# Kernel tuning notes

Measured on AMD Instinct MI355X. Metric: run time of the kernel, lower is better.

Reference implementation:

```python
import jax, jax.numpy as jnp
import numpy as np

D_MODEL = 1024
N_HEADS = 16
D_HEAD = D_MODEL // N_HEADS  # 64
M = int(round(D_HEAD * np.log(D_HEAD)))  # 266 random features, per source
KERNEL_EPS = 1e-4


def setup_inputs() -> dict:
    key = jax.random.key(0)
    ks = jax.random.split(key, 12)
    B, L = 2, 2048
    sc = 1.0 / np.sqrt(D_MODEL)
    return {
        "query": jax.random.normal(ks[0], (B, L, D_MODEL), jnp.float32),
        "key_": jax.random.normal(ks[1], (B, L, D_MODEL), jnp.float32),
        "value": jax.random.normal(ks[2], (B, L, D_MODEL), jnp.float32),
        "Wq": jax.random.normal(ks[3], (D_MODEL, D_MODEL), jnp.float32) * sc,
        "bq": jnp.zeros((D_MODEL,), jnp.float32),
        "Wk": jax.random.normal(ks[4], (D_MODEL, D_MODEL), jnp.float32) * sc,
        "bk": jnp.zeros((D_MODEL,), jnp.float32),
        "Wv": jax.random.normal(ks[5], (D_MODEL, D_MODEL), jnp.float32) * sc,
        "bv": jnp.zeros((D_MODEL,), jnp.float32),
        "Wo": jax.random.normal(ks[6], (D_MODEL, D_MODEL), jnp.float32) * sc,
        "bo": jnp.zeros((D_MODEL,), jnp.float32),
        "random_features": jax.random.normal(ks[7], (M, D_HEAD), jnp.float32),
    }


def _split_heads(x):
    # [B,L,d_model] -> [B,H,L,D]
    B, L, _ = x.shape
    return x.reshape(B, L, N_HEADS, D_HEAD).transpose(0, 2, 1, 3)


def _favor_projected(q, k, rf):
    # q,k: [B,H,L,D]; rf: [M,D]. Faithful to get_projected_queries_and_keys (kernel_type='exp').
    q = q / (D_MODEL ** 0.25)
    k = k / (D_MODEL ** 0.25)
    pq = jnp.einsum('bhld,md->bhlm', q, rf)
    pk = jnp.einsum('bhld,md->bhlm', k, rf)
    h_q = -0.5 * jnp.sum(q * q, axis=-1, keepdims=True)  # [B,H,L,1]
    h_k = -0.5 * jnp.sum(k * k, axis=-1, keepdims=True)
    q_stab = jnp.max(h_q, axis=-1, keepdims=True)  # == h_q (last dim is 1), as in source
    k_stab = jnp.max(h_k)  # global scalar, as in source
    q_ker = jnp.exp(h_q + (pq - q_stab))
    k_ker = jnp.exp(h_k + (pk - k_stab))
    c = M ** (-0.5)
    return c * (q_ker + KERNEL_EPS), c * (k_ker + KERNEL_EPS)


def _causal_favor(qp, kp, v):
    # qp,kp: [L,B,H,M]; v: [L,B,H,D]. Prefix-sum linear attention.
    # Denominator: q_prime[i] . cumsum(k_prime)[i]
    denom = jnp.einsum('lbhm,lbhm->lbh', qp, jnp.cumsum(kp, axis=0))

    # Numerator: recurrent scan carrying S = sum_j k'_j v_j^T  ([B,H,M,D])
    def step(S, inp):
        q_t, k_t, v_t = inp
        S = S + k_t[..., :, None] * v_t[..., None, :]
        out_t = jnp.einsum('bhmd,bhm->bhd', S, q_t)
        return S, out_t

    S0 = jnp.zeros(kp.shape[1:] + (v.shape[-1],), kp.dtype)
    _, num = jax.lax.scan(step, S0, (qp, kp, v))  # num: [L,B,H,D]
    return num / denom[..., None]


def reference(query, key_, value, Wq, bq, Wk, bk, Wv, bv, Wo, bo, random_features):
    B, L, _ = query.shape
    q = _split_heads(query @ Wq + bq)   # [B,H,L,D]
    k = _split_heads(key_ @ Wk + bk)
    v = _split_heads(value @ Wv + bv)
    q_prime, k_prime = _favor_projected(q, k, random_features)  # [B,H,L,M]
    # Causal path operates sequence-first: [L,B,H,*]
    qp = q_prime.transpose(2, 0, 1, 3)
    kp = k_prime.transpose(2, 0, 1, 3)
    vt = v.transpose(2, 0, 1, 3)
    out = _causal_favor(qp, kp, vt)               # [L,B,H,D]
    ctx = out.transpose(1, 0, 2, 3).reshape(B, L, D_MODEL)
    return ctx @ Wo + bo
```

## Files before the change

kernel.cpp:

```cpp
#include <hip/hip_runtime.h>
#include <hip/hip_bf16.h>

#define BATCH 2
#define SEQ 2048
#define DMODEL 1024
#define NH 16
#define HD 64
#define NRF 266
#define NRFP 288
#define CHK 128
#define NCH 16
#define NBH 32
#define NROWS 4096

constexpr float SCAL = 0.17677669529663687f;
constexpr float SCAL2 = 0.03125f;
constexpr float LN_CNORM = -2.7917480361965505f;
constexpr float CKEPS = 6.131393094576169e-6f;

typedef short bf16x8 __attribute__((ext_vector_type(8)));
typedef float f32x4 __attribute__((ext_vector_type(4)));

__device__ __forceinline__ short f2bs(float v) {
  __hip_bfloat16 h = __float2bfloat16(v);
  return *reinterpret_cast<short*>(&h);
}
__device__ __forceinline__ float bs2f(short s) {
  __hip_bfloat16 h;
  *reinterpret_cast<short*>(&h) = s;
  return __bfloat162float(h);
}
__device__ __forceinline__ void gload_lds16(const void* g, void* l) {
  __builtin_amdgcn_global_load_lds(
      (const __attribute__((address_space(1))) void*)g,
      (__attribute__((address_space(3))) void*)l, 16, 0, 0);
}
__device__ __forceinline__ unsigned f2ord(float f) {
  unsigned u = __float_as_uint(f);
  return (u & 0x80000000u) ? ~u : (u | 0x80000000u);
}
__device__ __forceinline__ float ord2f(unsigned e) {
  return (e & 0x80000000u) ? __uint_as_float(e & 0x7fffffffu)
                           : __uint_as_float(~e);
}

__global__ __launch_bounds__(256) void cvt3_kernel(const float* __restrict__ q,
                                                   const float* __restrict__ k,
                                                   const float* __restrict__ v,
                                                   short* __restrict__ out) {
  int z = blockIdx.y;
  const float* x = (z == 0) ? q : (z == 1) ? k : v;
  short* y = out + (size_t)z * NROWS * DMODEL;
  int i = (blockIdx.x * 256 + threadIdx.x) * 8;
  float4 a = *(const float4*)&x[i];
  float4 b = *(const float4*)&x[i + 4];
  bf16x8 o;
  o[0] = f2bs(a.x); o[1] = f2bs(a.y); o[2] = f2bs(a.z); o[3] = f2bs(a.w);
  o[4] = f2bs(b.x); o[5] = f2bs(b.y); o[6] = f2bs(b.z); o[7] = f2bs(b.w);
  *(bf16x8*)&y[i] = o;
}

__global__ __launch_bounds__(256) void rf_pad_bf16(const float* __restrict__ rf,
                                                   short* __restrict__ rfb,
                                                   unsigned* __restrict__ kord) {
  int idx = blockIdx.x * 256 + threadIdx.x;
  rfb[idx] = (idx < NRF * HD) ? f2bs(rf[idx] * SCAL) : (short)0;
  if (idx == 0) *kord = 0u;
}

__global__ __launch_bounds__(256) void transpose4_bf16(
    const float* __restrict__ Wq, const float* __restrict__ Wk,
    const float* __restrict__ Wv, const float* __restrict__ Wo,
    short* __restrict__ WtBase) {
  __shared__ float t[32][33];
  int z = blockIdx.z;
  const float* W = (z == 0) ? Wq : (z == 1) ? Wk : (z == 2) ? Wv : Wo;
  short* Wt = WtBase + (size_t)z * DMODEL * DMODEL;
  int k0 = blockIdx.y << 5, n0 = blockIdx.x << 5;
  int tx = threadIdx.x & 31, ty = threadIdx.x >> 5;
#pragma unroll
  for (int rr = 0; rr < 4; ++rr) {
    int r = ty + (rr << 3);
    t[r][tx] = W[(size_t)(k0 + r) * DMODEL + n0 + tx];
  }
  __syncthreads();
#pragma unroll
  for (int rr = 0; rr < 4; ++rr) {
    int r = ty + (rr << 3);
    Wt[(size_t)(n0 + r) * DMODEL + k0 + tx] = f2bs(t[tx][r]);
  }
}

template <bool OUTBF>
__device__ __forceinline__ void gemm_core128(const short* __restrict__ A,
                                             const short* __restrict__ Bt,
                                             const float* __restrict__ bias,
                                             void* __restrict__ C, int bm, int bn) {
  __shared__ short As[2][128 * 64];
  __shared__ short Bs[2][128 * 64];
  int tid = threadIdx.x;
  int lane = tid & 63, wid = tid >> 6;
  int wr = wid >> 1, wc = wid & 1;
  int cl = lane & 15, rq = lane >> 4;
  f32x4 acc[4][4];
#pragma unroll
  for (int m = 0; m < 4; ++m)
#pragma unroll
    for (int n = 0; n < 4; ++n) acc[m][n] = f32x4{0.f, 0.f, 0.f, 0.f};

  auto stage = [&](int buf, int k0) {
#pragma unroll
    for (int i = 0; i < 4; ++i) {
      int e = tid * 8 + i * 2048;
      int row = e >> 6;
      int k = (e & 63) ^ ((row & 7) << 3);
      gload_lds16(A + (size_t)(bm + row) * DMODEL + k0 + k,
                  &As[buf][wid * 512 + i * 2048]);
    }
#pragma unroll
    for (int i = 0; i < 4; ++i) {
      int e = tid * 8 + i * 2048;
      int row = e >> 6;
      int k = (e & 63) ^ ((row & 7) << 3);
      gload_lds16(Bt + (size_t)(bn + row) * DMODEL + k0 + k,
                  &Bs[buf][wid * 512 + i * 2048]);
    }
  };

  stage(0, 0);
#pragma unroll 2
  for (int t = 0; t < 16; ++t) {
    int cur = t & 1;
    if (t < 15) {
      stage(cur ^ 1, (t + 1) * 64);
      asm volatile("s_waitcnt vmcnt(8)" ::: "memory");
    } else {
      asm volatile("s_waitcnt vmcnt(0)" ::: "memory");
    }
    __builtin_amdgcn_s_barrier();
    asm volatile("" ::: "memory");
    const short* curA = &As[cur][0];
    const short* curB = &Bs[cur][0];
#pragma unroll
    for (int ks = 0; ks < 2; ++ks) {
      int kb = ks * 32 + (rq << 3);
      bf16x8 af[4], bfv[4];
#pragma unroll
      for (int mf = 0; mf < 4; ++mf) {
        int row = wr * 64 + mf * 16 + cl;
        af[mf] = *(const bf16x8*)&curA[row * 64 + (kb ^ ((row & 7) << 3))];
      }
#pragma unroll
      for (int nf = 0; nf < 4; ++nf) {
        int row = wc * 64 + nf * 16 + cl;
        bfv[nf] = *(const bf16x8*)&curB[row * 64 + (kb ^ ((row & 7) << 3))];
      }
#pragma unroll
      for (int mf = 0; mf < 4; ++mf)
#pragma unroll
        for (int nf = 0; nf < 4; ++nf)
          acc[mf][nf] = __builtin_amdgcn_mfma_f32_16x16x32_bf16(af[mf], bfv[nf],
                                                                acc[mf][nf], 0, 0, 0);
    }
    __builtin_amdgcn_s_barrier();
    asm volatile("" ::: "memory");
  }
  int rbase = bm + wr * 64 + (rq << 2);
  int cbase = bn + wc * 64 + cl;
#pragma unroll
  for (int nf = 0; nf < 4; ++nf) {
    int col = cbase + nf * 16;
    float bv = bias[col];
#pragma unroll
    for (int mf = 0; mf < 4; ++mf)
#pragma unroll
      for (int r = 0; r < 4; ++r) {
        int row = rbase + mf * 16 + r;
        float v = acc[mf][nf][r] + bv;
        if (OUTBF)
          ((short*)C)[(size_t)row * DMODEL + col] = f2bs(v);
        else
          ((float*)C)[(size_t)row * DMODEL + col] = v;
      }
  }
}

template <bool OUTBF>
__device__ __forceinline__ void gemm_core64(const short* __restrict__ A,
                                            const short* __restrict__ Bt,
                                            const float* __restrict__ bias,
                                            void* __restrict__ C, int bm, int bn) {
  __shared__ short As[2][128 * 64];
  __shared__ short Bs[2][64 * 64];
  int tid = threadIdx.x;
  int lane = tid & 63, wid = tid >> 6;
  int wr = wid >> 1, wc = wid & 1;
  f32x4 acc[4][2];
#pragma unroll
  for (int m = 0; m < 4; ++m)
#pragma unroll
    for (int n = 0; n < 2; ++n) acc[m][n] = f32x4{0.f, 0.f, 0.f, 0.f};

  auto stage = [&](int buf, int k0) {
#pragma unroll
    for (int i = 0; i < 4; ++i) {
      int e = tid * 8 + i * 2048;
      int row = e >> 6;
      int k = (e & 63) ^ ((row & 7) << 3);
      gload_lds16(A + (size_t)(bm + row) * DMODEL + k0 + k,
                  &As[buf][wid * 512 + i * 2048]);
    }
#pragma unroll
    for (int i = 0; i < 2; ++i) {
      int e = tid * 8 + i * 2048;
      int row = e >> 6;
      int k = (e & 63) ^ ((row & 7) << 3);
      gload_lds16(Bt + (size_t)(bn + row) * DMODEL + k0 + k,
                  &Bs[buf][wid * 512 + i * 2048]);
    }
  };

  stage(0, 0);
#pragma unroll 2
  for (int t = 0; t < 16; ++t) {
    int cur = t & 1;
    if (t < 15) {
      stage(cur ^ 1, (t + 1) * 64);
      asm volatile("s_waitcnt vmcnt(6)" ::: "memory");
    } else {
      asm volatile("s_waitcnt vmcnt(0)" ::: "memory");
    }
    __builtin_amdgcn_s_barrier();
    asm volatile("" ::: "memory");
    const short* curA = &As[cur][0];
    const short* curB = &Bs[cur][0];
#pragma unroll
    for (int ks = 0; ks < 2; ++ks) {
      int kb = ks * 32 + ((lane >> 4) << 3);
      bf16x8 af[4], bfv[2];
#pragma unroll
      for (int mf = 0; mf < 4; ++mf) {
        int row = wr * 64 + mf * 16 + (lane & 15);
        af[mf] = *(const bf16x8*)&curA[row * 64 + (kb ^ ((row & 7) << 3))];
      }
#pragma unroll
      for (int nf = 0; nf < 2; ++nf) {
        int row = wc * 32 + nf * 16 + (lane & 15);
        bfv[nf] = *(const bf16x8*)&curB[row * 64 + (kb ^ ((row & 7) << 3))];
      }
#pragma unroll
      for (int mf = 0; mf < 4; ++mf)
#pragma unroll
        for (int nf = 0; nf < 2; ++nf)
          acc[mf][nf] = __builtin_amdgcn_mfma_f32_16x16x32_bf16(af[mf], bfv[nf],
                                                                acc[mf][nf], 0, 0, 0);
    }
    __builtin_amdgcn_s_barrier();
    asm volatile("" ::: "memory");
  }
  int rbase = bm + wr * 64 + ((lane >> 4) << 2);
  int cbase = bn + wc * 32 + (lane & 15);
#pragma unroll
  for (int nf = 0; nf < 2; ++nf) {
    int col = cbase + nf * 16;
    float bv = bias[col];
#pragma unroll
    for (int mf = 0; mf < 4; ++mf)
#pragma unroll
      for (int r = 0; r < 4; ++r) {
        int row = rbase + mf * 16 + r;
        float v = acc[mf][nf][r] + bv;
        if (OUTBF)
          ((short*)C)[(size_t)row * DMODEL + col] = f2bs(v);
        else
          ((float*)C)[(size_t)row * DMODEL + col] = v;
      }
  }
}

__global__ __launch_bounds__(256) void gemm_qkv3(
    const short* __restrict__ Abase, const short* __restrict__ WtBase,
    const float* __restrict__ bq, const float* __restrict__ bk,
    const float* __restrict__ bv, short* __restrict__ OutBase) {
  int z = blockIdx.z;
  const short* A = Abase + (size_t)z * NROWS * DMODEL;
  const short* Bt = WtBase + (size_t)z * DMODEL * DMODEL;
  const float* bias = (z == 0) ? bq : (z == 1) ? bk : bv;
  short* C = OutBase + (size_t)z * NROWS * DMODEL;
  int bid = blockIdx.x + (blockIdx.y << 3);
  int swz = ((bid & 7) << 5) + (bid >> 3);
  int bn = (swz & 7) << 7;
  int bm = (swz >> 3) << 7;
  gemm_core128<true>(A, Bt, bias, C, bm, bn);
}

__global__ __launch_bounds__(256) void gemm_out(const short* __restrict__ A,
                                                const short* __restrict__ Bt,
                                                const float* __restrict__ bias,
                                                float* __restrict__ C) {
  int bid = blockIdx.x + (blockIdx.y << 4);
  int swz = ((bid & 7) << 6) + (bid >> 3);
  int bn = (swz & 15) << 6;
  int bm = (swz >> 4) << 7;
  gemm_core64<false>(A, Bt, bias, C, bm, bn);
}

__global__ __launch_bounds__(256) void hk_kernel(const short* __restrict__ Kb,
                                                 float* __restrict__ hkbuf,
                                                 unsigned* __restrict__ kord) {
  int tid = threadIdx.x;
  int rloc = tid >> 4, h = tid & 15;
  int n = blockIdx.x * 16 + rloc;
  const short* p = Kb + (size_t)n * DMODEL + h * HD;
  float ss = 0.f;
#pragma unroll
  for (int g = 0; g < 8; ++g) {
    bf16x8 v = *(const bf16x8*)(p + g * 8);
#pragma unroll
    for (int e = 0; e < 8; ++e) {
      float x = bs2f(v[e]);
      ss += x * x;
    }
  }
  float hkv = -0.5f * SCAL2 * ss;
  int b = n >> 11, l = n & (SEQ - 1);
  hkbuf[((size_t)(b * NH + h)) * SEQ + l] = hkv;
  __shared__ float red[256];
  red[tid] = hkv;
  __syncthreads();
  for (int s = 128; s > 0; s >>= 1) {
    if (tid < s) red[tid] = fmaxf(red[tid], red[tid + s]);
    __syncthreads();
  }
  if (tid == 0) atomicMax(kord, f2ord(red[0]));
}

__global__ __launch_bounds__(256, 1) void featmap_mfma(
    const short* __restrict__ Qproj, const short* __restrict__ Kproj,
    const short* __restrict__ rfb, const float* __restrict__ hkbuf,
    const unsigned* __restrict__ kord, short* __restrict__ Qp,
    short* __restrict__ Kp) {
  __shared__ short smem[26624];
  __shared__ float hks[128];
  short* As = smem;
  short* Bs = smem + 8192;
  int isK = blockIdx.z;
  const short* X = isK ? Kproj : Qproj;
  short* O = isK ? Kp : Qp;
  int bh = blockIdx.y, b = bh >> 4, h = bh & 15;
  int l0 = blockIdx.x << 7;
  int tid = threadIdx.x, lane = tid & 63, wid = tid >> 6;
  int cl = lane & 15, rq = lane >> 4;

#pragma unroll
  for (int i = 0; i < 4; ++i) {
    int e = tid * 8 + i * 2048;
    int row = e >> 6;
    int k = (e & 63) ^ ((row & 7) << 3);
    gload_lds16(X + ((size_t)b * SEQ + l0 + row) * DMODEL + h * HD + k,
                &As[wid * 512 + i * 2048]);
  }
#pragma unroll
  for (int i = 0; i < 9; ++i) {
    int e = tid * 8 + i * 2048;
    int row = e >> 6;
    int k = (e & 63) ^ ((row & 7) << 3);
    gload_lds16(rfb + row * HD + k, &Bs[wid * 512 + i * 2048]);
  }
  if (isK) {
    float ksv = ord2f(*kord);
    if (tid < 128)
      hks[tid] = hkbuf[(size_t)bh * SEQ + l0 + tid] - ksv + LN_CNORM;
  }
  __syncthreads();

  int i0 = wid * 32;
  f32x4 acc[2][18];
#pragma unroll
  for (int m = 0; m < 2; ++m)
#pragma unroll
    for (int n = 0; n < 18; ++n) acc[m][n] = f32x4{0.f, 0.f, 0.f, 0.f};
#pragma unroll
  for (int ks = 0; ks < 2; ++ks) {
    int kb = ks * 32 + (rq << 3);
    int swz = (cl & 7) << 3;
    bf16x8 af[2];
#pragma unroll
    for (int mf = 0; mf < 2; ++mf) {
      int row = i0 + mf * 16 + cl;
      af[mf] = *(const bf16x8*)&As[row * 64 + (kb ^ swz)];
    }
#pragma unroll
    for (int nf = 0; nf < 18; ++nf) {
      int brow = nf * 16 + cl;
      bf16x8 bv = *(const bf16x8*)&Bs[brow * 64 + (kb ^ swz)];
#pragma unroll
      for (int mf = 0; mf < 2; ++mf)
        acc[mf][nf] = __builtin_amdgcn_mfma_f32_16x16x32_bf16(af[mf], bv,
                                                              acc[mf][nf], 0, 0, 0);
    }
  }

  short* Ps = smem;
#pragma unroll
  for (int hf = 0; hf < 2; ++hf) {
    __syncthreads();
#pragma unroll
    for (int mf = 0; mf < 2; ++mf)
#pragma unroll
      for (int r = 0; r < 4; ++r) {
        int rl = i0 + mf * 16 + (rq << 2) + r;
        float addk = isK ? hks[rl] : LN_CNORM;
#pragma unroll
        for (int nf2 = 0; nf2 < 9; ++nf2) {
          int m = hf * 144 + nf2 * 16 + cl;
          float v = acc[mf][hf * 9 + nf2][r] + addk;
          float o = (m < NRF) ? (__expf(v) + CKEPS) : 0.f;
          Ps[rl * 152 + nf2 * 16 + cl] = f2bs(o);
        }
      }
    __syncthreads();
#pragma unroll
    for (int it = 0; it < 9; ++it) {
      int idx = tid + it * 256;
      int row = idx / 18, ch = idx - row * 18;
      bf16x8 val = *(const bf16x8*)&Ps[row * 152 + ch * 8];
      *(bf16x8*)&O[((size_t)bh * SEQ + l0 + row) * NRFP + hf * 144 + ch * 8] = val;
    }
  }
}

__global__ __launch_bounds__(256) void chunksum_mfma(
    const short* __restrict__ Kp, const short* __restrict__ Vb,
    short* __restrict__ Schunk, float* __restrict__ ksum) {
  constexpr int ST = 70;
  __shared__ short KT[NRFP * ST];
  __shared__ short VT[HD * ST];
  int c = blockIdx.x, bh = blockIdx.y;
  int b = bh >> 4, h = bh & 15;
  int tid = threadIdx.x, lane = tid & 63, wv = tid >> 6;
  int cl = lane & 15, rq = lane >> 4;
  int irow = tid >> 2;
  int mq = tid & 3;
  size_t rowb = (size_t)bh * SEQ + (size_t)c * CHK;

  f32x4 acc[18];
#pragma unroll
  for (int m = 0; m < 18; ++m) acc[m] = f32x4{0.f, 0.f, 0.f, 0.f};
  float k1 = 0.f, k2 = 0.f;

  for (int hf = 0; hf < 2; ++hf) {
    __syncthreads();
    const short* Krow = Kp + (rowb + hf * 64 + irow) * NRFP;
#pragma unroll
    for (int cg = 0; cg < 9; ++cg) {
      int m0 = cg * 32 + mq * 8;
      bf16x8 v = *(const bf16x8*)(Krow + m0);
#pragma unroll
      for (int e = 0; e < 8; ++e) KT[(m0 + e) * ST + irow] = v[e];
    }
    const short* Vrow =
        Vb + ((size_t)b * SEQ + (size_t)c * CHK + hf * 64 + irow) * DMODEL + h * HD;
    {
      int d0 = mq * 16;
      bf16x8 v0 = *(const bf16x8*)(Vrow + d0);
      bf16x8 v1 = *(const bf16x8*)(Vrow + d0 + 8);
#pragma unroll
      for (int e = 0; e < 8; ++e) VT[(d0 + e) * ST + irow] = v0[e];
#pragma unroll
      for (int e = 0; e < 8; ++e) VT[(d0 + 8 + e) * ST + irow] = v1[e];
    }
    __syncthreads();
#pragma unroll
    for (int ks = 0; ks < 2; ++ks) {
      int kb = ks * 32 + rq * 8;
      bf16x8 bv = *(const bf16x8*)&VT[(wv * 16 + cl) * ST + kb];
#pragma unroll
      for (int mf = 0; mf < 18; ++mf) {
        bf16x8 av = *(const bf16x8*)&KT[(mf * 16 + cl) * ST + kb];
        acc[mf] = __builtin_amdgcn_mfma_f32_16x16x32_bf16(av, bv, acc[mf], 0, 0, 0);
      }
    }
    {
      const short* r1 = &KT[tid * ST];
#pragma unroll
      for (int g = 0; g < 8; ++g) {
        bf16x8 v = *(const bf16x8*)(r1 + g * 8);
#pragma unroll
        for (int e = 0; e < 8; ++e) k1 += bs2f(v[e]);
      }
      if (tid < 10) {
        const short* r2 = &KT[(256 + tid) * ST];
#pragma unroll
        for (int g = 0; g < 8; ++g) {
          bf16x8 v = *(const bf16x8*)(r2 + g * 8);
#pragma unroll
          for (int e = 0; e < 8; ++e) k2 += bs2f(v[e]);
        }
      }
    }
  }
  size_t sbase = ((size_t)bh * NCH + c) * (size_t)(NRFP * HD);
  size_t kbase = ((size_t)bh * NCH + c) * (size_t)NRF;
#pragma unroll
  for (int mf = 0; mf < 18; ++mf)
#pragma unroll
    for (int r = 0; r < 4; ++r) {
      int m = mf * 16 + rq * 4 + r;
      Schunk[sbase + (size_t)m * HD + wv * 16 + cl] = f2bs(acc[mf][r]);
    }
  if (tid < NRF) ksum[kbase + tid] = k1;
  if (tid < 10) ksum[kbase + 256 + tid] = k2;
}

__global__ __launch_bounds__(256) void prefix_all(const short* __restrict__ Sc,
                                                  short* __restrict__ Sp,
                                                  float* __restrict__ ksum) {
  int bh = blockIdx.y;
  if (blockIdx.x == 72) {
    for (int m = threadIdx.x; m < NRF; m += 256) {
      size_t base = (size_t)bh * NCH * NRF + m;
      float a = 0.f;
#pragma unroll
      for (int c = 0; c < NCH; ++c) {
        size_t idx = base + (size_t)c * NRF;
        float v = ksum[idx];
        ksum[idx] = a;
        a += v;
      }
    }
    return;
  }
  int e = blockIdx.x * 256 + threadIdx.x;
  size_t base = (size_t)bh * NCH * (NRFP * HD) + e;
  float a = 0.f;
#pragma unroll
  for (int c = 0; c < NCH; ++c) {
    size_t idx = base + (size_t)c * (NRFP * HD);
    float v = bs2f(Sc[idx]);
    Sp[idx] = f2bs(a);
    a += v;
  }
}

__global__ __launch_bounds__(256) void attn_mfma(
    const short* __restrict__ Qp, const short* __restrict__ Kp,
    const short* __restrict__ Vb, const short* __restrict__ Sp,
    const float* __restrict__ ksum, short* __restrict__ ctxb) {
  constexpr int PST = 136;
  constexpr int BST = 290;
  __shared__ short Vt[64 * PST];
  __shared__ short BsPl[64 * BST];
  __shared__ float ks[272];
  __shared__ float den[128];
  int c = blockIdx.x, bh = blockIdx.y;
  int b = bh >> 4, h = bh & 15;
  int tid = threadIdx.x, lane = tid & 63, wid = tid >> 6;
  int cl = lane & 15, rq = lane >> 4;
  size_t rowb = (size_t)bh * SEQ + (size_t)c * CHK;

  {
    int jj = tid >> 3, d0 = (tid & 7) << 3;
#pragma unroll
    for (int jt = 0; jt < 4; ++jt) {
      int j = jj + jt * 32;
      bf16x8 v = *(const bf16x8*)(Vb + ((size_t)b * SEQ + (size_t)c * CHK + j) * DMODEL +
                                  h * HD + d0);
#pragma unroll
      for (int e = 0; e < 8; ++e) Vt[(d0 + e) * PST + j] = v[e];
    }
  }
  const short* Spb = Sp + ((size_t)bh * NCH + c) * (size_t)(NRFP * HD);
  for (int idx = tid; idx < NRFP * HD; idx += 256) {
    int m = idx >> 6, d = idx & 63;
    BsPl[d * BST + m] = Spb[idx];
  }
  const float* ksb = ksum + ((size_t)bh * NCH + c) * (size_t)NRF;
  for (int idx = tid; idx < NRF; idx += 256) ks[idx] = ksb[idx];
  __syncthreads();

  int i0 = wid * 32;
  const short* Arow = Qp + (rowb + i0) * NRFP;
  const short* Krow = Kp + rowb * NRFP;
  f32x4 accI[2][4];
  f32x4 accP[2][8];
#pragma unroll
  for (int m = 0; m < 2; ++m) {
#pragma unroll
    for (int n = 0; n < 4; ++n) accI[m][n] = f32x4{0.f, 0.f, 0.f, 0.f};
#pragma unroll
    for (int n = 0; n < 8; ++n) accP[m][n] = f32x4{0.f, 0.f, 0.f, 0.f};
  }
#pragma unroll
  for (int k9 = 0; k9 < 9; ++k9) {
    int kb = k9 * 32 + (rq << 3);
    bf16x8 af[2];
#pragma unroll
    for (int mf = 0; mf < 2; ++mf)
      af[mf] = *(const bf16x8*)(Arow + (size_t)(mf * 16 + cl) * NRFP + kb);
#pragma unroll
    for (int nf = 0; nf < 4; ++nf) {
      bf16x8 bv = *(const bf16x8*)&BsPl[(nf * 16 + cl) * BST + kb];
#pragma unroll
      for (int mf = 0; mf < 2; ++mf)
        accI[mf][nf] = __builtin_amdgcn_mfma_f32_16x16x32_bf16(af[mf], bv,
                                                               accI[mf][nf], 0, 0, 0);
    }
#pragma unroll
    for (int nf = 0; nf < 8; ++nf) {
      bf16x8 bv = *(const bf16x8*)(Krow + (size_t)(nf * 16 + cl) * NRFP + kb);
#pragma unroll
      for (int mf = 0; mf < 2; ++mf)
        accP[mf][nf] = __builtin_amdgcn_mfma_f32_16x16x32_bf16(af[mf], bv,
                                                               accP[mf][nf], 0, 0, 0);
    }
  }
  {
    int r = tid >> 1, half = tid & 1;
    const short* qr = Qp + (rowb + r) * NRFP;
    float s = 0.f;
    int m0 = half * 133;
    for (int m = m0; m < m0 + 133; ++m) s += bs2f(qr[m]) * ks[m];
    s += __shfl_xor(s, 1);
    if (!half) den[r] = s;
  }
  __syncthreads();

#pragma unroll
  for (int mf = 0; mf < 2; ++mf)
#pragma unroll
    for (int r = 0; r < 4; ++r) {
      int rl = mf * 16 + (rq << 2) + r;
      int row = i0 + rl;
      float dsum = 0.f;
#pragma unroll
      for (int nf = 0; nf < 8; ++nf) {
        int col = nf * 16 + cl;
        float v = (col > row) ? 0.f : accP[mf][nf][r];
        dsum += v;
        BsPl[wid * 32 * PST + rl * PST + col] = f2bs(v);
      }
      dsum += __shfl_xor(dsum, 1);
      dsum += __shfl_xor(dsum, 2);
      dsum += __shfl_xor(dsum, 4);
      dsum += __shfl_xor(dsum, 8);
      if (cl == 0) den[row] += dsum;
    }
  __syncthreads();

  f32x4 pacc[2][4];
#pragma unroll
  for (int m = 0; m < 2; ++m)
#pragma unroll
    for (int n = 0; n < 4; ++n) pacc[m][n] = f32x4{0.f, 0.f, 0.f, 0.f};
#pragma unroll
  for (int kk = 0; kk < 4; ++kk) {
    int kb = kk * 32 + (rq << 3);
    bf16x8 paf[2];
#pragma unroll
    for (int mf = 0; mf < 2; ++mf)
      paf[mf] = *(const bf16x8*)&BsPl[wid * 32 * PST + (mf * 16 + cl) * PST + kb];
#pragma unroll
    for (int nf = 0; nf < 4; ++nf) {
      bf16x8 bv = *(const bf16x8*)&Vt[(nf * 16 + cl) * PST + kb];
#pragma unroll
      for (int mf = 0; mf < 2; ++mf)
        pacc[mf][nf] = __builtin_amdgcn_mfma_f32_16x16x32_bf16(paf[mf], bv,
                                                               pacc[mf][nf], 0, 0, 0);
    }
  }
#pragma unroll
  for (int mf = 0; mf < 2; ++mf)
#pragma unroll
    for (int r = 0; r < 4; ++r) {
      int row = i0 + mf * 16 + (rq << 2) + r;
      float inv = 1.0f / den[row];
      size_t ob = ((size_t)b * SEQ + (size_t)c * CHK + row) * DMODEL + h * HD;
#pragma unroll
      for (int nf = 0; nf < 4; ++nf) {
        int d = nf * 16 + cl;
        float v = (accI[mf][nf][r] + pacc[mf][nf][r]) * inv;
        ctxb[ob + d] = f2bs(v);
      }
    }
}

extern "C" void kernel_launch(void* const* d_in, const int* in_sizes, int n_in,
                              void* d_out, int out_size, void* d_ws, size_t ws_size,
                              hipStream_t stream) {
  (void)in_sizes; (void)n_in; (void)out_size;
  const float* query = (const float*)d_in[0];
  const float* key_  = (const float*)d_in[1];
  const float* value = (const float*)d_in[2];
  const float* Wq = (const float*)d_in[3];
  const float* bq = (const float*)d_in[4];
  const float* Wk = (const float*)d_in[5];
  const float* bk = (const float*)d_in[6];
  const float* Wv = (const float*)d_in[7];
  const float* bv = (const float*)d_in[8];
  const float* Wo = (const float*)d_in[9];
  const float* bo = (const float*)d_in[10];
  const float* rf = (const float*)d_in[11];

  constexpr size_t SZ_INBF = (size_t)NROWS * DMODEL * 2;
  constexpr size_t SZ_QP   = (size_t)NBH * SEQ * NRFP * 2;
  constexpr size_t SZ_WT   = (size_t)DMODEL * DMODEL * 2;
  constexpr size_t SZ_SCH  = (size_t)NBH * NCH * NRFP * HD * 2;
  constexpr size_t SZ_KS   = (size_t)NBH * NCH * NRF * 4;
  constexpr size_t SZ_HK   = (size_t)NBH * SEQ * 4;
  constexpr size_t SZ_RFB  = (size_t)NRFP * HD * 2;

  constexpr size_t O_QP   = 0;
  constexpr size_t O_KP   = O_QP + SZ_QP;
  constexpr size_t O_WT   = O_KP + SZ_QP;
  constexpr size_t O_QPR  = O_WT + 4 * SZ_WT;
  constexpr size_t O_SCH  = O_QPR + 3 * SZ_INBF;
  constexpr size_t O_SPR  = O_SCH + SZ_SCH;
  constexpr size_t O_KSUM = O_SPR + SZ_SCH;
  constexpr size_t O_HK   = O_KSUM + SZ_KS;
  constexpr size_t O_KST  = O_HK + SZ_HK;
  constexpr size_t O_CTXB = O_KST + 256;
  constexpr size_t O_RFB  = O_CTXB + SZ_INBF;
  constexpr size_t O_END  = O_RFB + SZ_RFB;
  if (ws_size < O_END) return;

  char* w = (char*)d_ws;
  short* Qbf  = (short*)(w + O_QP);
  short* Qp   = (short*)(w + O_QP);
  short* Kp   = (short*)(w + O_KP);
  short* WtB  = (short*)(w + O_WT);
  short* QprB = (short*)(w + O_QPR);
  short* Kpr  = (short*)(w + O_QPR + SZ_INBF);
  short* Vpr  = (short*)(w + O_QPR + 2 * SZ_INBF);
  short* Sch  = (short*)(w + O_SCH);
  short* Spr  = (short*)(w + O_SPR);
  float* ksum = (float*)(w + O_KSUM);
  float* hkbuf = (float*)(w + O_HK);
  unsigned* kord = (unsigned*)(w + O_KST);
  short* ctxb = (short*)(w + O_CTXB);
  short* rfb  = (short*)(w + O_RFB);

  constexpr int NEL = NROWS * DMODEL;
  cvt3_kernel<<<dim3(NEL / 2048, 3), 256, 0, stream>>>(query, key_, value, Qbf);
  transpose4_bf16<<<dim3(32, 32, 4), 256, 0, stream>>>(Wq, Wk, Wv, Wo, WtB);
  rf_pad_bf16<<<(NRFP * HD) / 256, 256, 0, stream>>>(rf, rfb, kord);
  gemm_qkv3<<<dim3(8, 32, 3), 256, 0, stream>>>(Qbf, WtB, bq, bk, bv, QprB);
  hk_kernel<<<256, 256, 0, stream>>>(Kpr, hkbuf, kord);
  featmap_mfma<<<dim3(SEQ / 128, NBH, 2), 256, 0, stream>>>(QprB, Kpr, rfb, hkbuf,
                                                            kord, Qp, Kp);
  chunksum_mfma<<<dim3(NCH, NBH), 256, 0, stream>>>(Kp, Vpr, Sch, ksum);
  prefix_all<<<dim3(73, NBH), 256, 0, stream>>>(Sch, Spr, ksum);
  attn_mfma<<<dim3(NCH, NBH), 256, 0, stream>>>(Qp, Kp, Vpr, Spr, ksum, ctxb);
  gemm_out<<<dim3(16, 32), 256, 0, stream>>>(ctxb, WtB + 3 * (size_t)DMODEL * DMODEL,
                                             bo, (float*)d_out);
}
```

Baseline: 184.7 us.

## Store chunk states transposed, async-load to swizzled LDS, compute denominator via MFMA

Result: no change. 184.1 us, median of 2 (-0.3%).

```diff
diff --git a/kernel.cpp b/kernel.cpp
--- a/kernel.cpp
+++ b/kernel.cpp
@@ -8,6 +8,7 @@
 #define HD 64
 #define NRF 266
 #define NRFP 288
+#define SROW 320
 #define CHK 128
 #define NCH 16
 #define NBH 32
@@ -432,7 +433,7 @@
 
 __global__ __launch_bounds__(256) void chunksum_mfma(
     const short* __restrict__ Kp, const short* __restrict__ Vb,
-    short* __restrict__ Schunk, float* __restrict__ ksum) {
+    short* __restrict__ Sct, float* __restrict__ ksum) {
   constexpr int ST = 70;
   __shared__ short KT[NRFP * ST];
   __shared__ short VT[HD * ST];
@@ -500,65 +501,81 @@
       }
     }
   }
-  size_t sbase = ((size_t)bh * NCH + c) * (size_t)(NRFP * HD);
+  size_t sbase = ((size_t)bh * NCH + c) * (size_t)(HD * SROW);
+  int d = wv * 16 + cl;
+#pragma unroll
+  for (int mf = 0; mf < 18; ++mf) {
+    short4 o4 = make_short4(f2bs(acc[mf][0]), f2bs(acc[mf][1]),
+                            f2bs(acc[mf][2]), f2bs(acc[mf][3]));
+    *(short4*)&Sct[sbase + (size_t)d * SROW + mf * 16 + rq * 4] = o4;
+  }
+  {
+    int dz = tid >> 2, off = NRFP + ((tid & 3) << 3);
+    bf16x8 z = {0, 0, 0, 0, 0, 0, 0, 0};
+    *(bf16x8*)&Sct[sbase + (size_t)dz * SROW + off] = z;
+  }
   size_t kbase = ((size_t)bh * NCH + c) * (size_t)NRF;
-#pragma unroll
-  for (int mf = 0; mf < 18; ++mf)
-#pragma unroll
-    for (int r = 0; r < 4; ++r) {
-      int m = mf * 16 + rq * 4 + r;
-      Schunk[sbase + (size_t)m * HD + wv * 16 + cl] = f2bs(acc[mf][r]);
-    }
   if (tid < NRF) ksum[kbase + tid] = k1;
   if (tid < 10) ksum[kbase + 256 + tid] = k2;
 }
 
-__global__ __launch_bounds__(256) void prefix_all(const short* __restrict__ Sc,
-                                                  short* __restrict__ Sp,
-                                                  float* __restrict__ ksum) {
+__global__ __launch_bounds__(256) void prefix_all(const short* __restrict__ Sct,
+                                                  short* __restrict__ Spt,
+                                                  const float* __restrict__ ksum,
+                                                  short* __restrict__ ksb) {
   int bh = blockIdx.y;
-  if (blockIdx.x == 72) {
-    for (int m = threadIdx.x; m < NRF; m += 256) {
-      size_t base = (size_t)bh * NCH * NRF + m;
-      float a = 0.f;
-#pragma unroll
-      for (int c = 0; c < NCH; ++c) {
-        size_t idx = base + (size_t)c * NRF;
-        float v = ksum[idx];
-        ksum[idx] = a;
-        a += v;
+  if (blockIdx.x == 80) {
+    for (int m = threadIdx.x; m < NRFP; m += 256) {
+      if (m < NRF) {
+        size_t base = (size_t)bh * NCH * NRF + m;
+        float a = 0.f;
+#pragma unroll
+        for (int c = 0; c < NCH; ++c) {
+          float v = ksum[base + (size_t)c * NRF];
+          ksb[((size_t)bh * NCH + c) * NRFP + m] = f2bs(a);
+          a += v;
+        }
+      } else {
+#pragma unroll
+        for (int c = 0; c < NCH; ++c)
+          ksb[((size_t)bh * NCH + c) * NRFP + m] = 0;
       }
     }
     return;
   }
   int e = blockIdx.x * 256 + threadIdx.x;
-  size_t base = (size_t)bh * NCH * (NRFP * HD) + e;
   float a = 0.f;
 #pragma unroll
   for (int c = 0; c < NCH; ++c) {
-    size_t idx = base + (size_t)c * (NRFP * HD);
-    float v = bs2f(Sc[idx]);
-    Sp[idx] = f2bs(a);
+    size_t idx = ((size_t)bh * NCH + c) * (size_t)(HD * SROW) + e;
+    float v = bs2f(Sct[idx]);
+    Spt[idx] = f2bs(a);
     a += v;
   }
 }
 
 __global__ __launch_bounds__(256) void attn_mfma(
     const short* __restrict__ Qp, const short* __restrict__ Kp,
-    const short* __restrict__ Vb, const short* __restrict__ Sp,
-    const float* __restrict__ ksum, short* __restrict__ ctxb) {
+    const short* __restrict__ Vb, const short* __restrict__ Spt,
+    const short* __restrict__ ksb, short* __restrict__ ctxb) {
   constexpr int PST = 136;
-  constexpr int BST = 290;
   __shared__ short Vt[64 * PST];
-  __shared__ short BsPl[64 * BST];
-  __shared__ float ks[272];
-  __shared__ float den[128];
+  __shared__ short SP[64 * SROW];
   int c = blockIdx.x, bh = blockIdx.y;
   int b = bh >> 4, h = bh & 15;
   int tid = threadIdx.x, lane = tid & 63, wid = tid >> 6;
   int cl = lane & 15, rq = lane >> 4;
   size_t rowb = (size_t)bh * SEQ + (size_t)c * CHK;
 
+  const short* sg = Spt + ((size_t)bh * NCH + c) * (size_t)(HD * SROW);
+#pragma unroll
+  for (int i = 0; i < 10; ++i) {
+    int o = tid * 8 + i * 2048;
+    int d = o / SROW;
+    int m = o - d * SROW;
+    int ms = m ^ ((d & 7) << 3);
+    gload_lds16(sg + (size_t)d * SROW + ms, &SP[wid * 512 + i * 2048]);
+  }
   {
     int jj = tid >> 3, d0 = (tid & 7) << 3;
 #pragma unroll
@@ -570,24 +587,20 @@
       for (int e = 0; e < 8; ++e) Vt[(d0 + e) * PST + j] = v[e];
     }
   }
-  const short* Spb = Sp + ((size_t)bh * NCH + c) * (size_t)(NRFP * HD);
-  for (int idx = tid; idx < NRFP * HD; idx += 256) {
-    int m = idx >> 6, d = idx & 63;
-    BsPl[d * BST + m] = Spb[idx];
-  }
-  const float* ksb = ksum + ((size_t)bh * NCH + c) * (size_t)NRF;
-  for (int idx = tid; idx < NRF; idx += 256) ks[idx] = ksb[idx];
   __syncthreads();
 
   int i0 = wid * 32;
   const short* Arow = Qp + (rowb + i0) * NRFP;
   const short* Krow = Kp + rowb * NRFP;
+  const short* krow = ksb + ((size_t)bh * NCH + c) * NRFP;
   f32x4 accI[2][4];
+  f32x4 accD[2];
   f32x4 accP[2][8];
 #pragma unroll
   for (int m = 0; m < 2; ++m) {
 #pragma unroll
     for (int n = 0; n < 4; ++n) accI[m][n] = f32x4{0.f, 0.f, 0.f, 0.f};
+    accD[m] = f32x4{0.f, 0.f, 0.f, 0.f};
 #pragma unroll
     for (int n = 0; n < 8; ++n) accP[m][n] = f32x4{0.f, 0.f, 0.f, 0.f};
   }
@@ -598,9 +611,15 @@
 #pragma unroll
     for (int mf = 0; mf < 2; ++mf)
       af[mf] = *(const bf16x8*)(Arow + (size_t)(mf * 16 + cl) * NRFP + kb);
+    bf16x8 bvD = {0, 0, 0, 0, 0, 0, 0, 0};
+    if (cl == 0) bvD = *(const bf16x8*)(krow + kb);
+#pragma unroll
+    for (int mf = 0; mf < 2; ++mf)
+      accD[mf] = __builtin_amdgcn_mfma_f32_16x16x32_bf16(af[mf], bvD, accD[mf], 0, 0, 0);
 #pragma unroll
     for (int nf = 0; nf < 4; ++nf) {
-      bf16x8 bv = *(const bf16x8*)&BsPl[(nf * 16 + cl) * BST + kb];
+      int row = nf * 16 + cl;
+      bf16x8 bv = *(const bf16x8*)&SP[row * SROW + (kb ^ ((cl & 7) << 3))];
 #pragma unroll
       for (int mf = 0; mf < 2; ++mf)
         accI[mf][nf] = __builtin_amdgcn_mfma_f32_16x16x32_bf16(af[mf], bv,
@@ -615,17 +634,9 @@
                                                                accP[mf][nf], 0, 0, 0);
     }
   }
-  {
-    int r = tid >> 1, half = tid & 1;
-    const short* qr = Qp + (rowb + r) * NRFP;
-    float s = 0.f;
-    int m0 = half * 133;
-    for (int m = m0; m < m0 + 133; ++m) s += bs2f(qr[m]) * ks[m];
-    s += __shfl_xor(s, 1);
-    if (!half) den[r] = s;
-  }
   __syncthreads();
 
+  float dtot[2][4];
 #pragma unroll
   for (int mf = 0; mf < 2; ++mf)
 #pragma unroll
@@ -638,13 +649,14 @@
         int col = nf * 16 + cl;
         float v = (col > row) ? 0.f : accP[mf][nf][r];
         dsum += v;
-        BsPl[wid * 32 * PST + rl * PST + col] = f2bs(v);
+        SP[wid * 32 * PST + rl * PST + col] = f2bs(v);
       }
       dsum += __shfl_xor(dsum, 1);
       dsum += __shfl_xor(dsum, 2);
       dsum += __shfl_xor(dsum, 4);
       dsum += __shfl_xor(dsum, 8);
-      if (cl == 0) den[row] += dsum;
+      float dden = __shfl(accD[mf][r], lane & 48);
+      dtot[mf][r] = dden + dsum;
     }
   __syncthreads();
 
@@ -659,7 +671,7 @@
     bf16x8 paf[2];
 #pragma unroll
     for (int mf = 0; mf < 2; ++mf)
-      paf[mf] = *(const bf16x8*)&BsPl[wid * 32 * PST + (mf * 16 + cl) * PST + kb];
+      paf[mf] = *(const bf16x8*)&SP[wid * 32 * PST + (mf * 16 + cl) * PST + kb];
 #pragma unroll
     for (int nf = 0; nf < 4; ++nf) {
       bf16x8 bv = *(const bf16x8*)&Vt[(nf * 16 + cl) * PST + kb];
@@ -674,7 +686,7 @@
 #pragma unroll
     for (int r = 0; r < 4; ++r) {
       int row = i0 + mf * 16 + (rq << 2) + r;
-      float inv = 1.0f / den[row];
+      float inv = 1.0f / dtot[mf][r];
       size_t ob = ((size_t)b * SEQ + (size_t)c * CHK + row) * DMODEL + h * HD;
 #pragma unroll
       for (int nf = 0; nf < 4; ++nf) {
@@ -705,8 +717,9 @@
   constexpr size_t SZ_INBF = (size_t)NROWS * DMODEL * 2;
   constexpr size_t SZ_QP   = (size_t)NBH * SEQ * NRFP * 2;
   constexpr size_t SZ_WT   = (size_t)DMODEL * DMODEL * 2;
-  constexpr size_t SZ_SCH  = (size_t)NBH * NCH * NRFP * HD * 2;
+  constexpr size_t SZ_SCH  = (size_t)NBH * NCH * HD * SROW * 2;
   constexpr size_t SZ_KS   = (size_t)NBH * NCH * NRF * 4;
+  constexpr size_t SZ_KSB  = (size_t)NBH * NCH * NRFP * 2;
   constexpr size_t SZ_HK   = (size_t)NBH * SEQ * 4;
   constexpr size_t SZ_RFB  = (size_t)NRFP * HD * 2;
 
@@ -717,7 +730,8 @@
   constexpr size_t O_SCH  = O_QPR + 3 * SZ_INBF;
   constexpr size_t O_SPR  = O_SCH + SZ_SCH;
   constexpr size_t O_KSUM = O_SPR + SZ_SCH;
-  constexpr size_t O_HK   = O_KSUM + SZ_KS;
+  constexpr size_t O_KSB  = O_KSUM + SZ_KS;
+  constexpr size_t O_HK   = O_KSB + SZ_KSB;
   constexpr size_t O_KST  = O_HK + SZ_HK;
   constexpr size_t O_CTXB = O_KST + 256;
   constexpr size_t O_RFB  = O_CTXB + SZ_INBF;
@@ -732,9 +746,10 @@
   short* QprB = (short*)(w + O_QPR);
   short* Kpr  = (short*)(w + O_QPR + SZ_INBF);
   short* Vpr  = (short*)(w + O_QPR + 2 * SZ_INBF);
-  short* Sch  = (short*)(w + O_SCH);
-  short* Spr  = (short*)(w + O_SPR);
+  short* Sct  = (short*)(w + O_SCH);
+  short* Spt  = (short*)(w + O_SPR);
   float* ksum = (float*)(w + O_KSUM);
+  short* ksb  = (short*)(w + O_KSB);
   float* hkbuf = (float*)(w + O_HK);
   unsigned* kord = (unsigned*)(w + O_KST);
   short* ctxb = (short*)(w + O_CTXB);
@@ -748,9 +763,9 @@
   hk_kernel<<<256, 256, 0, stream>>>(Kpr, hkbuf, kord);
   featmap_mfma<<<dim3(SEQ / 128, NBH, 2), 256, 0, stream>>>(QprB, Kpr, rfb, hkbuf,
                                                             kord, Qp, Kp);
-  chunksum_mfma<<<dim3(NCH, NBH), 256, 0, stream>>>(Kp, Vpr, Sch, ksum);
-  prefix_all<<<dim3(73, NBH), 256, 0, stream>>>(Sch, Spr, ksum);
-  attn_mfma<<<dim3(NCH, NBH), 256, 0, stream>>>(Qp, Kp, Vpr, Spr, ksum, ctxb);
+  chunksum_mfma<<<dim3(NCH, NBH), 256, 0, stream>>>(Kp, Vpr, Sct, ksum);
+  prefix_all<<<dim3(81, NBH), 256, 0, stream>>>(Sct, Spt, ksum, ksb);
+  attn_mfma<<<dim3(NCH, NBH), 256, 0, stream>>>(Qp, Kp, Vpr, Spt, ksb, ctxb);
   gemm_out<<<dim3(16, 32), 256, 0, stream>>>(ctxb, WtB + 3 * (size_t)DMODEL * DMODEL,
                                              bo, (float*)d_out);
 }
```
